# Kernel tuning notes

Hardware: AMD Instinct MI355X
Metric: run time of the kernel (lower is better)

The kernel has to match this reference:

```python
import jax, jax.numpy as jnp
import numpy as np

B, S, H, C = 8, 4096, 768, 64  # batch, seq_len, hidden_dim, block size


def _xavier(k, shape):
    fan = shape[0] + shape[1]
    return jax.random.normal(k, shape, jnp.float32) * np.sqrt(2.0 / fan)


def setup_inputs() -> dict:
    key = jax.random.key(0)
    kx, kq, kk, kv, k1, k2 = jax.random.split(key, 6)
    return {
        "x": jax.random.normal(kx, (B, S, H), jnp.float32),
        "Wq": _xavier(kq, (H, H)),
        "Wk": _xavier(kk, (H, H)),
        "Wv": _xavier(kv, (H, H)),
        "W1": _xavier(k1, (H, 16)),
        "W2": _xavier(k2, (16, H)),
        "b": jnp.zeros((H,), jnp.float32),
    }


def reference(x, Wq, Wk, Wv, W1, W2, b):
    Bb, Ss, Hh = x.shape
    NB = Ss // C  # number of blocks (seq_len divisible by C, no remainder)
    Q = x @ Wq
    K = x @ Wk
    V = x @ Wv
    # gating alpha: identical every block iteration in the original, compute once
    alpha = jax.nn.sigmoid((x @ W1) @ W2 + b) ** (1.0 / 16.0)  # [B,S,H]
    a = alpha.mean(axis=1, keepdims=True)  # [B,1,H], broadcasts over rows of state
    # blocks to leading axis for scan: [NB, B, C, H]
    qs = Q.reshape(Bb, NB, C, Hh).transpose(1, 0, 2, 3)
    ks = K.reshape(Bb, NB, C, Hh).transpose(1, 0, 2, 3)
    vs = V.reshape(Bb, NB, C, Hh).transpose(1, 0, 2, 3)
    mask = jnp.tril(jnp.ones((C, C), x.dtype))
    scale = 1.0 / np.sqrt(Hh).astype(np.float32)

    def step(St, blk):
        qb, kb, vb = blk  # each [B,C,H]
        # state update first (original updates S before computing output)
        St = St * a + jnp.einsum("bch,bcd->bhd", kb, vb)  # [B,H,H]
        # intra-block: scores masked by MULTIPLICATION (as in original), then softmax
        scores = jnp.einsum("bch,bdh->bcd", qb, kb) * mask * scale
        w = jax.nn.softmax(scores, axis=-1)
        out = jnp.einsum("bch,bhd->bcd", qb, St) + jnp.einsum("bcd,bde->bce", w, vb)
        return St, out

    S0 = jnp.zeros((Bb, Hh, Hh), x.dtype)
    _, outs = jax.lax.scan(step, S0, (qs, ks, vs))  # outs: [NB,B,C,H]
    O = outs.transpose(1, 0, 2, 3).reshape(Bb, Ss, Hh)
    return O
```

## Files before the change

kernel.cpp:

```cpp
#include <hip/hip_runtime.h>

#define B_ 8
#define S_ 4096
#define H_ 768
#define C_ 64
#define NB_ 64
#define M_ (B_*S_)

typedef _Float16 f16x8 __attribute__((ext_vector_type(8)));
typedef _Float16 f16x4 __attribute__((ext_vector_type(4)));
typedef float    f32x4 __attribute__((ext_vector_type(4)));

__global__ __launch_bounds__(256) void k_transpose(const float* __restrict__ src,
                                                   _Float16* __restrict__ dst) {
  __shared__ float tile[32][33];
  const int t = threadIdx.x;
  const int tx = t & 31, ty = t >> 5;
  const int n0 = blockIdx.x * 32, k0 = blockIdx.y * 32;
#pragma unroll
  for (int i = 0; i < 4; ++i)
    tile[ty + i*8][tx] = src[(k0 + ty + i*8) * H_ + n0 + tx];
  __syncthreads();
#pragma unroll
  for (int i = 0; i < 4; ++i)
    dst[(n0 + ty + i*8) * H_ + k0 + tx] = (_Float16)tile[tx][ty + i*8];
}

__global__ __launch_bounds__(256) void k_gemm_qkv(
    const float* __restrict__ x,
    const _Float16* __restrict__ WqT, const _Float16* __restrict__ WkT,
    const _Float16* __restrict__ WvT,
    _Float16* __restrict__ Qb, _Float16* __restrict__ Vb,
    _Float16* __restrict__ KT, _Float16* __restrict__ VT) {
  __shared__ _Float16 xs[64][40];
  __shared__ _Float16 ws[3][128][40];
  const int t = threadIdx.x;
  const int m0 = blockIdx.x * 64, n0 = blockIdx.y * 128;
  const int lane = t & 63, wv = t >> 6;
  const int lm = lane & 15, qd = lane >> 4;
  const int sm = t >> 2, sk = (t & 3) * 8;
  const int wn = t >> 1, wk = (t & 1) * 16;

  f32x4 acc[3][4][2];
#pragma unroll
  for (int a = 0; a < 3; ++a)
#pragma unroll
    for (int i = 0; i < 4; ++i)
#pragma unroll
      for (int n = 0; n < 2; ++n)
        acc[a][i][n] = (f32x4){0.f, 0.f, 0.f, 0.f};

  for (int kk = 0; kk < 24; ++kk) {
    const int k0 = kk * 32;
    __syncthreads();
    {
      const f32x4* xp = (const f32x4*)&x[(size_t)(m0 + sm) * H_ + k0 + sk];
      f32x4 f0 = xp[0], f1 = xp[1];
      f16x8 xv;
#pragma unroll
      for (int j = 0; j < 4; ++j) { xv[j] = (_Float16)f0[j]; xv[4 + j] = (_Float16)f1[j]; }
      *(f16x8*)&xs[sm][sk] = xv;
    }
    {
      const f16x8* wp = (const f16x8*)&WqT[(n0 + wn) * H_ + k0 + wk];
      *(f16x8*)&ws[0][wn][wk] = wp[0]; *(f16x8*)&ws[0][wn][wk + 8] = wp[1];
      wp = (const f16x8*)&WkT[(n0 + wn) * H_ + k0 + wk];
      *(f16x8*)&ws[1][wn][wk] = wp[0]; *(f16x8*)&ws[1][wn][wk + 8] = wp[1];
      wp = (const f16x8*)&WvT[(n0 + wn) * H_ + k0 + wk];
      *(f16x8*)&ws[2][wn][wk] = wp[0]; *(f16x8*)&ws[2][wn][wk + 8] = wp[1];
    }
    __syncthreads();
    f16x8 af[4];
#pragma unroll
    for (int i = 0; i < 4; ++i) af[i] = *(f16x8*)&xs[i*16 + lm][qd*8];
#pragma unroll
    for (int a = 0; a < 3; ++a)
#pragma unroll
      for (int n = 0; n < 2; ++n) {
        f16x8 bfr = *(f16x8*)&ws[a][wv*32 + n*16 + lm][qd*8];
#pragma unroll
        for (int i = 0; i < 4; ++i)
          acc[a][i][n] = __builtin_amdgcn_mfma_f32_16x16x32_f16(af[i], bfr, acc[a][i][n], 0, 0, 0);
      }
  }
#pragma unroll
  for (int i = 0; i < 4; ++i)
#pragma unroll
    for (int n = 0; n < 2; ++n) {
      const int ng = n0 + wv*32 + n*16 + lm;
      const int mg0 = m0 + i*16 + qd*4;
      const int bb = mg0 >> 12, ss = mg0 & (S_ - 1);
#pragma unroll
      for (int r = 0; r < 4; ++r) {
        Qb[(size_t)(mg0 + r) * H_ + ng] = (_Float16)acc[0][i][n][r];
        Vb[(size_t)(mg0 + r) * H_ + ng] = (_Float16)acc[2][i][n][r];
      }
      f16x4 kp, vp;
#pragma unroll
      for (int r = 0; r < 4; ++r) {
        kp[r] = (_Float16)acc[1][i][n][r];
        vp[r] = (_Float16)acc[2][i][n][r];
      }
      *(f16x4*)&KT[((size_t)bb * H_ + ng) * S_ + ss] = kp;
      *(f16x4*)&VT[((size_t)bb * H_ + ng) * S_ + ss] = vp;
    }
}

__global__ __launch_bounds__(256) void k_tgemm(const float* __restrict__ x,
                                               const float* __restrict__ W1,
                                               float* __restrict__ tbuf) {
  __shared__ float w1s[768 * 16];
  __shared__ float xs[64 * 129];
  const int t = threadIdx.x;
  const int m0 = blockIdx.x * 64;
  for (int i = t; i < 768 * 16 / 4; i += 256)
    ((f32x4*)w1s)[i] = ((const f32x4*)W1)[i];
  const int row = t & 63, cg = t >> 6;
  f32x4 acc = (f32x4){0.f, 0.f, 0.f, 0.f};
  for (int kc = 0; kc < 768; kc += 128) {
    __syncthreads();
    for (int i = 0; i < 32; ++i) {
      const int idx = t + 256 * i;
      const int r = idx >> 7, c = idx & 127;
      xs[r * 129 + c] = x[(size_t)(m0 + r) * H_ + kc + c];
    }
    __syncthreads();
#pragma unroll 8
    for (int kl = 0; kl < 128; ++kl) {
      const float a = xs[row * 129 + kl];
      const f32x4 w = *(const f32x4*)&w1s[(kc + kl) * 16 + cg * 4];
#pragma unroll
      for (int j = 0; j < 4; ++j) acc[j] += a * w[j];
    }
  }
  *(f32x4*)&tbuf[(size_t)(m0 + row) * 16 + cg * 4] = acc;
}

__global__ __launch_bounds__(256) void k_areduce(const float* __restrict__ tbuf,
                                                 const float* __restrict__ W2,
                                                 const float* __restrict__ bias,
                                                 float* __restrict__ abuf) {
  __shared__ float ts[128 * 17];
  __shared__ float rbuf[8 * 32];
  const int t = threadIdx.x;
  const int b = blockIdx.y, hc = blockIdx.x;
  const int hl = t & 31, sg = t >> 5;
  const int h = hc * 32 + hl;
  float w2r[16];
#pragma unroll
  for (int j = 0; j < 16; ++j) w2r[j] = W2[j * H_ + h];
  const float bb = bias[h];
  float asum = 0.f;
  const float* tb = &tbuf[(size_t)(b * S_) * 16];
  for (int sc = 0; sc < S_; sc += 128) {
    __syncthreads();
    for (int i = 0; i < 8; ++i) {
      const int idx = t + 256 * i;
      const int sl = idx >> 4, j = idx & 15;
      ts[sl * 17 + j] = tb[(size_t)(sc + sl) * 16 + j];
    }
    __syncthreads();
    for (int i = 0; i < 16; ++i) {
      const int sl = sg + i * 8;
      float z = bb;
      const float* tr = &ts[sl * 17];
#pragma unroll
      for (int j = 0; j < 16; ++j) z += tr[j] * w2r[j];
      const float sgm = 1.f / (1.f + __expf(-z));
      asum += sqrtf(sqrtf(sqrtf(sqrtf(sgm))));
    }
  }
  rbuf[sg * 32 + hl] = asum;
  __syncthreads();
  if (t < 32) {
    float s = 0.f;
#pragma unroll
    for (int g = 0; g < 8; ++g) s += rbuf[g * 32 + t];
    abuf[b * H_ + hc * 32 + t] = s * (1.f / (float)S_);
  }
}

__global__ __launch_bounds__(256) void k_scores_y(
    const _Float16* __restrict__ Qb, const _Float16* __restrict__ KT,
    const _Float16* __restrict__ Vb, float* __restrict__ O) {
  __shared__ float qs[64 * 68];
  __shared__ float ks[64 * 68];
  __shared__ float wb[64 * 68];
  __shared__ float vsb[64 * 68];
  const int t = threadIdx.x;
  const int nb = blockIdx.x, b = blockIdx.y;
  const size_t base = ((size_t)b * S_ + nb * 64) * H_;
  const int tc = t >> 4, td = t & 15;
  const int srow = t >> 2, sseg = (t & 3) * 16;

  float scr[4][4];
#pragma unroll
  for (int i = 0; i < 4; ++i)
#pragma unroll
    for (int u = 0; u < 4; ++u) scr[i][u] = 0.f;

  for (int hc = 0; hc < 12; ++hc) {
    __syncthreads();
    {
      const f16x8* qp = (const f16x8*)&Qb[base + (size_t)srow * H_ + hc * 64 + sseg];
      f16x8 q0 = qp[0], q1 = qp[1];
#pragma unroll
      for (int j = 0; j < 8; ++j) {
        qs[(sseg + j) * 68 + srow] = (float)q0[j];
        qs[(sseg + 8 + j) * 68 + srow] = (float)q1[j];
      }
    }
    {
      const size_t krow = ((size_t)b * H_ + hc * 64 + srow) * S_ + nb * 64 + sseg;
      f16x8 k0 = *(const f16x8*)&KT[krow];
      f16x8 k1 = *(const f16x8*)&KT[krow + 8];
      f32x4 f;
#pragma unroll
      for (int j = 0; j < 4; ++j) f[j] = (float)k0[j];
      *(f32x4*)&ks[srow * 68 + sseg] = f;
#pragma unroll
      for (int j = 0; j < 4; ++j) f[j] = (float)k0[4 + j];
      *(f32x4*)&ks[srow * 68 + sseg + 4] = f;
#pragma unroll
      for (int j = 0; j < 4; ++j) f[j] = (float)k1[j];
      *(f32x4*)&ks[srow * 68 + sseg + 8] = f;
#pragma unroll
      for (int j = 0; j < 4; ++j) f[j] = (float)k1[4 + j];
      *(f32x4*)&ks[srow * 68 + sseg + 12] = f;
    }
    __syncthreads();
#pragma unroll 4
    for (int h = 0; h < 64; ++h) {
      const f32x4 qv = *(f32x4*)&qs[h * 68 + tc * 4];
      const f32x4 kv = *(f32x4*)&ks[h * 68 + td * 4];
#pragma unroll
      for (int i = 0; i < 4; ++i)
#pragma unroll
        for (int u = 0; u < 4; ++u) scr[i][u] += qv[i] * kv[u];
    }
  }
  const float scale = 0.036084391824351615f;
#pragma unroll
  for (int i = 0; i < 4; ++i)
#pragma unroll
    for (int u = 0; u < 4; ++u) {
      const int c = tc * 4 + i, d = td * 4 + u;
      wb[d * 68 + c] = (d <= c) ? scr[i][u] * scale : 0.f;
    }
  __syncthreads();
  {
    const int r = t >> 2, g = t & 3;
    float vals[16];
    float mx = -1e30f;
#pragma unroll
    for (int i = 0; i < 16; ++i) {
      vals[i] = wb[(g * 16 + i) * 68 + r];
      mx = fmaxf(mx, vals[i]);
    }
    mx = fmaxf(mx, __shfl_xor(mx, 1));
    mx = fmaxf(mx, __shfl_xor(mx, 2));
    float sm = 0.f;
#pragma unroll
    for (int i = 0; i < 16; ++i) { vals[i] = __expf(vals[i] - mx); sm += vals[i]; }
    sm += __shfl_xor(sm, 1);
    sm += __shfl_xor(sm, 2);
    const float inv = 1.f / sm;
#pragma unroll
    for (int i = 0; i < 16; ++i) wb[(g * 16 + i) * 68 + r] = vals[i] * inv;
  }
  for (int ec = 0; ec < 12; ++ec) {
    __syncthreads();
    {
      const f16x8* vp = (const f16x8*)&Vb[base + (size_t)srow * H_ + ec * 64 + sseg];
      f16x8 v0 = vp[0], v1 = vp[1];
      f32x4 f;
#pragma unroll
      for (int j = 0; j < 4; ++j) f[j] = (float)v0[j];
      *(f32x4*)&vsb[srow * 68 + sseg] = f;
#pragma unroll
      for (int j = 0; j < 4; ++j) f[j] = (float)v0[4 + j];
      *(f32x4*)&vsb[srow * 68 + sseg + 4] = f;
#pragma unroll
      for (int j = 0; j < 4; ++j) f[j] = (float)v1[j];
      *(f32x4*)&vsb[srow * 68 + sseg + 8] = f;
#pragma unroll
      for (int j = 0; j < 4; ++j) f[j] = (float)v1[4 + j];
      *(f32x4*)&vsb[srow * 68 + sseg + 12] = f;
    }
    __syncthreads();
    float y[4][4];
#pragma unroll
    for (int i = 0; i < 4; ++i)
#pragma unroll
      for (int u = 0; u < 4; ++u) y[i][u] = 0.f;
#pragma unroll 4
    for (int j = 0; j < 64; ++j) {
      const f32x4 wv = *(f32x4*)&wb[j * 68 + tc * 4];
      const f32x4 vv = *(f32x4*)&vsb[j * 68 + td * 4];
#pragma unroll
      for (int i = 0; i < 4; ++i)
#pragma unroll
        for (int u = 0; u < 4; ++u) y[i][u] += wv[i] * vv[u];
    }
#pragma unroll
    for (int i = 0; i < 4; ++i) {
      f32x4 yv = {y[i][0], y[i][1], y[i][2], y[i][3]};
      *(f32x4*)&O[base + (size_t)(tc * 4 + i) * H_ + ec * 64 + td * 4] = yv;
    }
  }
}

#define STP 776
__global__ __launch_bounds__(256, 2) void k_scan(
    const _Float16* __restrict__ Qb, const _Float16* __restrict__ KT,
    const _Float16* __restrict__ VT, const float* __restrict__ abuf,
    float* __restrict__ O) {
  __shared__ _Float16 StL[32 * STP];
  const int t = threadIdx.x;
  const int b = blockIdx.y;
  const int d0 = blockIdx.x * 32;
  const int w = t >> 6, lane = t & 63;
  const int lm = lane & 15, qd = lane >> 4;

  const float av0 = abuf[b * H_ + d0 + lm];
  const float av1 = abuf[b * H_ + d0 + 16 + lm];

  f32x4 acc[12][2];
#pragma unroll
  for (int mt = 0; mt < 12; ++mt) {
    acc[mt][0] = (f32x4){0.f, 0.f, 0.f, 0.f};
    acc[mt][1] = (f32x4){0.f, 0.f, 0.f, 0.f};
  }

  const size_t ktb = (size_t)b * H_ * S_;
  const size_t vrow0 = ktb + (size_t)(d0 + lm) * S_;
  const size_t vrow1 = ktb + (size_t)(d0 + 16 + lm) * S_;

  for (int blk = 0; blk < NB_; ++blk) {
    const int s0 = blk * 64;
    f16x8 vf00 = *(const f16x8*)&VT[vrow0 + s0 + qd * 8];
    f16x8 vf01 = *(const f16x8*)&VT[vrow0 + s0 + 32 + qd * 8];
    f16x8 vf10 = *(const f16x8*)&VT[vrow1 + s0 + qd * 8];
    f16x8 vf11 = *(const f16x8*)&VT[vrow1 + s0 + 32 + qd * 8];
#pragma unroll
    for (int mt = 0; mt < 12; ++mt) {
      const size_t arow = ktb + (size_t)((w * 12 + mt) * 16 + lm) * S_ + s0 + qd * 8;
      f16x8 a0 = *(const f16x8*)&KT[arow];
      f16x8 a1 = *(const f16x8*)&KT[arow + 32];
      f32x4 c0 = acc[mt][0] * av0;
      f32x4 c1 = acc[mt][1] * av1;
      c0 = __builtin_amdgcn_mfma_f32_16x16x32_f16(a0, vf00, c0, 0, 0, 0);
      c0 = __builtin_amdgcn_mfma_f32_16x16x32_f16(a1, vf01, c0, 0, 0, 0);
      c1 = __builtin_amdgcn_mfma_f32_16x16x32_f16(a0, vf10, c1, 0, 0, 0);
      c1 = __builtin_amdgcn_mfma_f32_16x16x32_f16(a1, vf11, c1, 0, 0, 0);
      acc[mt][0] = c0;
      acc[mt][1] = c1;
    }
    __syncthreads();
#pragma unroll
    for (int mt = 0; mt < 12; ++mt) {
      const int h = (w * 12 + mt) * 16 + qd * 4;
      f16x4 p0, p1;
#pragma unroll
      for (int r = 0; r < 4; ++r) {
        p0[r] = (_Float16)acc[mt][0][r];
        p1[r] = (_Float16)acc[mt][1][r];
      }
      *(f16x4*)&StL[lm * STP + h] = p0;
      *(f16x4*)&StL[(16 + lm) * STP + h] = p1;
    }
    __syncthreads();
    f32x4 o0a = {0.f,0.f,0.f,0.f}, o0b = {0.f,0.f,0.f,0.f};
    f32x4 o1a = {0.f,0.f,0.f,0.f}, o1b = {0.f,0.f,0.f,0.f};
    const size_t qrow = ((size_t)b * S_ + s0 + w * 16 + lm) * H_ + qd * 8;
#pragma unroll 3
    for (int kt = 0; kt < 24; kt += 2) {
      f16x8 qa = *(const f16x8*)&Qb[qrow + kt * 32];
      f16x8 qb2 = *(const f16x8*)&Qb[qrow + kt * 32 + 32];
      f16x8 s00 = *(f16x8*)&StL[lm * STP + kt * 32 + qd * 8];
      f16x8 s01 = *(f16x8*)&StL[(16 + lm) * STP + kt * 32 + qd * 8];
      f16x8 s10 = *(f16x8*)&StL[lm * STP + kt * 32 + 32 + qd * 8];
      f16x8 s11 = *(f16x8*)&StL[(16 + lm) * STP + kt * 32 + 32 + qd * 8];
      o0a = __builtin_amdgcn_mfma_f32_16x16x32_f16(qa, s00, o0a, 0, 0, 0);
      o1a = __builtin_amdgcn_mfma_f32_16x16x32_f16(qa, s01, o1a, 0, 0, 0);
      o0b = __builtin_amdgcn_mfma_f32_16x16x32_f16(qb2, s10, o0b, 0, 0, 0);
      o1b = __builtin_amdgcn_mfma_f32_16x16x32_f16(qb2, s11, o1b, 0, 0, 0);
    }
    const f32x4 o0 = o0a + o0b;
    const f32x4 o1 = o1a + o1b;
    const size_t orow = ((size_t)b * S_ + s0 + w * 16 + qd * 4) * H_ + d0;
#pragma unroll
    for (int r = 0; r < 4; ++r) {
      O[orow + (size_t)r * H_ + lm] += o0[r];
      O[orow + (size_t)r * H_ + 16 + lm] += o1[r];
    }
  }
}

extern "C" void kernel_launch(void* const* d_in, const int* in_sizes, int n_in,
                              void* d_out, int out_size, void* d_ws, size_t ws_size,
                              hipStream_t stream) {
  (void)in_sizes; (void)n_in; (void)out_size; (void)ws_size;
  const float* x    = (const float*)d_in[0];
  const float* Wq   = (const float*)d_in[1];
  const float* Wk   = (const float*)d_in[2];
  const float* Wv   = (const float*)d_in[3];
  const float* W1   = (const float*)d_in[4];
  const float* W2   = (const float*)d_in[5];
  const float* bias = (const float*)d_in[6];
  float* O = (float*)d_out;

  char* ws = (char*)d_ws;
  _Float16* Qb  = (_Float16*)ws;
  _Float16* Vb  = Qb + (size_t)M_ * H_;
  _Float16* KT  = Vb + (size_t)M_ * H_;
  _Float16* VT  = KT + (size_t)M_ * H_;
  _Float16* WqT = VT + (size_t)M_ * H_;
  _Float16* WkT = WqT + H_ * H_;
  _Float16* WvT = WkT + H_ * H_;
  float* tbuf = (float*)(WvT + H_ * H_);
  float* abuf = tbuf + (size_t)M_ * 16;

  k_transpose<<<dim3(24, 24), 256, 0, stream>>>(Wq, WqT);
  k_transpose<<<dim3(24, 24), 256, 0, stream>>>(Wk, WkT);
  k_transpose<<<dim3(24, 24), 256, 0, stream>>>(Wv, WvT);
  k_gemm_qkv<<<dim3(512, 6), 256, 0, stream>>>(x, WqT, WkT, WvT, Qb, Vb, KT, VT);
  k_tgemm<<<dim3(512), 256, 0, stream>>>(x, W1, tbuf);
  k_areduce<<<dim3(24, 8), 256, 0, stream>>>(tbuf, W2, bias, abuf);
  k_scores_y<<<dim3(64, 8), 256, 0, stream>>>(Qb, KT, Vb, O);
  k_scan<<<dim3(24, 8), 256, 0, stream>>>(Qb, KT, VT, abuf, O);
}
```

Before: 1.534 ms.

## Split sequential state scan into parallel chunks with carry combine pass

The serial 64-block state scan, which ran on only 192 workgroups, is replaced by a three-phase chunked scan. Each of 8 chunks first computes its local state contribution in parallel. A combine kernel then propagates carries using a^8 decay, and a final pass recomputes each chunk's outputs starting from its carried-in state. This raises parallelism eightfold for the bottleneck kernel, at the cost of reading K and V twice and storing fp16 partial states. The row-major V copy is also dropped, and scores_y now reads and transposes from VT.

New measurement: 1.449 ms. 1.06x faster.

```diff
diff --git a/kernel.cpp b/kernel.cpp
--- a/kernel.cpp
+++ b/kernel.cpp
@@ -7,6 +7,9 @@
 #define NB_ 64
 #define M_ (B_*S_)
 
+#define NCH_ 8
+#define LCH_ 8
+
 typedef _Float16 f16x8 __attribute__((ext_vector_type(8)));
 typedef _Float16 f16x4 __attribute__((ext_vector_type(4)));
 typedef float    f32x4 __attribute__((ext_vector_type(4)));
@@ -30,7 +33,7 @@
     const float* __restrict__ x,
     const _Float16* __restrict__ WqT, const _Float16* __restrict__ WkT,
     const _Float16* __restrict__ WvT,
-    _Float16* __restrict__ Qb, _Float16* __restrict__ Vb,
+    _Float16* __restrict__ Qb,
     _Float16* __restrict__ KT, _Float16* __restrict__ VT) {
   __shared__ _Float16 xs[64][40];
   __shared__ _Float16 ws[3][128][40];
@@ -91,10 +94,8 @@
       const int mg0 = m0 + i*16 + qd*4;
       const int bb = mg0 >> 12, ss = mg0 & (S_ - 1);
 #pragma unroll
-      for (int r = 0; r < 4; ++r) {
+      for (int r = 0; r < 4; ++r)
         Qb[(size_t)(mg0 + r) * H_ + ng] = (_Float16)acc[0][i][n][r];
-        Vb[(size_t)(mg0 + r) * H_ + ng] = (_Float16)acc[2][i][n][r];
-      }
       f16x4 kp, vp;
 #pragma unroll
       for (int r = 0; r < 4; ++r) {
@@ -182,7 +183,7 @@
 
 __global__ __launch_bounds__(256) void k_scores_y(
     const _Float16* __restrict__ Qb, const _Float16* __restrict__ KT,
-    const _Float16* __restrict__ Vb, float* __restrict__ O) {
+    const _Float16* __restrict__ VT, float* __restrict__ O) {
   __shared__ float qs[64 * 68];
   __shared__ float ks[64 * 68];
   __shared__ float wb[64 * 68];
@@ -271,21 +272,14 @@
   for (int ec = 0; ec < 12; ++ec) {
     __syncthreads();
     {
-      const f16x8* vp = (const f16x8*)&Vb[base + (size_t)srow * H_ + ec * 64 + sseg];
-      f16x8 v0 = vp[0], v1 = vp[1];
-      f32x4 f;
-#pragma unroll
-      for (int j = 0; j < 4; ++j) f[j] = (float)v0[j];
-      *(f32x4*)&vsb[srow * 68 + sseg] = f;
-#pragma unroll
-      for (int j = 0; j < 4; ++j) f[j] = (float)v0[4 + j];
-      *(f32x4*)&vsb[srow * 68 + sseg + 4] = f;
-#pragma unroll
-      for (int j = 0; j < 4; ++j) f[j] = (float)v1[j];
-      *(f32x4*)&vsb[srow * 68 + sseg + 8] = f;
-#pragma unroll
-      for (int j = 0; j < 4; ++j) f[j] = (float)v1[4 + j];
-      *(f32x4*)&vsb[srow * 68 + sseg + 12] = f;
+      const size_t vrow = ((size_t)b * H_ + ec * 64 + srow) * S_ + nb * 64 + sseg;
+      f16x8 v0 = *(const f16x8*)&VT[vrow];
+      f16x8 v1 = *(const f16x8*)&VT[vrow + 8];
+#pragma unroll
+      for (int j = 0; j < 8; ++j) {
+        vsb[(sseg + j) * 68 + srow] = (float)v0[j];
+        vsb[(sseg + 8 + j) * 68 + srow] = (float)v1[j];
+      }
     }
     __syncthreads();
     float y[4][4];
@@ -310,15 +304,12 @@
   }
 }
 
-#define STP 776
-__global__ __launch_bounds__(256, 2) void k_scan(
-    const _Float16* __restrict__ Qb, const _Float16* __restrict__ KT,
-    const _Float16* __restrict__ VT, const float* __restrict__ abuf,
-    float* __restrict__ O) {
-  __shared__ _Float16 StL[32 * STP];
-  const int t = threadIdx.x;
-  const int b = blockIdx.y;
-  const int d0 = blockIdx.x * 32;
+__global__ __launch_bounds__(256, 2) void k_scan_chunk(
+    const _Float16* __restrict__ KT, const _Float16* __restrict__ VT,
+    const float* __restrict__ abuf, _Float16* __restrict__ Tb) {
+  const int t = threadIdx.x;
+  const int b = blockIdx.z, ch = blockIdx.y, dt = blockIdx.x;
+  const int d0 = dt * 32;
   const int w = t >> 6, lane = t & 63;
   const int lm = lane & 15, qd = lane >> 4;
 
@@ -336,7 +327,105 @@
   const size_t vrow0 = ktb + (size_t)(d0 + lm) * S_;
   const size_t vrow1 = ktb + (size_t)(d0 + 16 + lm) * S_;
 
-  for (int blk = 0; blk < NB_; ++blk) {
+  for (int blk = ch * LCH_; blk < ch * LCH_ + LCH_; ++blk) {
+    const int s0 = blk * 64;
+    f16x8 vf00 = *(const f16x8*)&VT[vrow0 + s0 + qd * 8];
+    f16x8 vf01 = *(const f16x8*)&VT[vrow0 + s0 + 32 + qd * 8];
+    f16x8 vf10 = *(const f16x8*)&VT[vrow1 + s0 + qd * 8];
+    f16x8 vf11 = *(const f16x8*)&VT[vrow1 + s0 + 32 + qd * 8];
+#pragma unroll
+    for (int mt = 0; mt < 12; ++mt) {
+      const size_t arow = ktb + (size_t)((w * 12 + mt) * 16 + lm) * S_ + s0 + qd * 8;
+      f16x8 a0 = *(const f16x8*)&KT[arow];
+      f16x8 a1 = *(const f16x8*)&KT[arow + 32];
+      f32x4 c0 = acc[mt][0] * av0;
+      f32x4 c1 = acc[mt][1] * av1;
+      c0 = __builtin_amdgcn_mfma_f32_16x16x32_f16(a0, vf00, c0, 0, 0, 0);
+      c0 = __builtin_amdgcn_mfma_f32_16x16x32_f16(a1, vf01, c0, 0, 0, 0);
+      c1 = __builtin_amdgcn_mfma_f32_16x16x32_f16(a0, vf10, c1, 0, 0, 0);
+      c1 = __builtin_amdgcn_mfma_f32_16x16x32_f16(a1, vf11, c1, 0, 0, 0);
+      acc[mt][0] = c0;
+      acc[mt][1] = c1;
+    }
+  }
+  _Float16* tp = Tb + ((((size_t)b * NCH_ + ch) * 24 + dt) * 32) * 768;
+#pragma unroll
+  for (int mt = 0; mt < 12; ++mt) {
+    const int h = (w * 12 + mt) * 16 + qd * 4;
+    f16x4 p0, p1;
+#pragma unroll
+    for (int r = 0; r < 4; ++r) {
+      p0[r] = (_Float16)acc[mt][0][r];
+      p1[r] = (_Float16)acc[mt][1][r];
+    }
+    *(f16x4*)&tp[(size_t)lm * 768 + h] = p0;
+    *(f16x4*)&tp[(size_t)(16 + lm) * 768 + h] = p1;
+  }
+}
+
+__global__ __launch_bounds__(256) void k_combine(const float* __restrict__ abuf,
+                                                 _Float16* __restrict__ Tb) {
+  const int gid = blockIdx.x * 256 + threadIdx.x;
+  const int hv = gid % 96;
+  const int dl = (gid / 96) & 31;
+  const int dt = (gid / (96 * 32)) % 24;
+  const int b  = gid / (96 * 32 * 24);
+  const float ad = abuf[b * H_ + dt * 32 + dl];
+  const float a2 = ad * ad, a4 = a2 * a2;
+  const float aL = a4 * a4;
+  float carry[8];
+#pragma unroll
+  for (int j = 0; j < 8; ++j) carry[j] = 0.f;
+  const size_t chstride = (size_t)24 * 32 * 768;
+  _Float16* p = Tb + (size_t)b * NCH_ * chstride + ((size_t)dt * 32 + dl) * 768 + hv * 8;
+  for (int ch = 0; ch < NCH_; ++ch, p += chstride) {
+    const f16x8 tv = *(const f16x8*)p;
+    f16x8 cv;
+#pragma unroll
+    for (int j = 0; j < 8; ++j) {
+      cv[j] = (_Float16)carry[j];
+      carry[j] = carry[j] * aL + (float)tv[j];
+    }
+    *(f16x8*)p = cv;
+  }
+}
+
+#define STP 776
+__global__ __launch_bounds__(256, 2) void k_scan_out(
+    const _Float16* __restrict__ Qb, const _Float16* __restrict__ KT,
+    const _Float16* __restrict__ VT, const float* __restrict__ abuf,
+    const _Float16* __restrict__ Tb, float* __restrict__ O) {
+  __shared__ _Float16 StL[32 * STP];
+  const int t = threadIdx.x;
+  const int b = blockIdx.z, ch = blockIdx.y, dt = blockIdx.x;
+  const int d0 = dt * 32;
+  const int w = t >> 6, lane = t & 63;
+  const int lm = lane & 15, qd = lane >> 4;
+
+  const float av0 = abuf[b * H_ + d0 + lm];
+  const float av1 = abuf[b * H_ + d0 + 16 + lm];
+
+  f32x4 acc[12][2];
+  {
+    const _Float16* tp = Tb + ((((size_t)b * NCH_ + ch) * 24 + dt) * 32) * 768;
+#pragma unroll
+    for (int mt = 0; mt < 12; ++mt) {
+      const int h = (w * 12 + mt) * 16 + qd * 4;
+      const f16x4 c0 = *(const f16x4*)&tp[(size_t)lm * 768 + h];
+      const f16x4 c1 = *(const f16x4*)&tp[(size_t)(16 + lm) * 768 + h];
+#pragma unroll
+      for (int r = 0; r < 4; ++r) {
+        acc[mt][0][r] = (float)c0[r];
+        acc[mt][1][r] = (float)c1[r];
+      }
+    }
+  }
+
+  const size_t ktb = (size_t)b * H_ * S_;
+  const size_t vrow0 = ktb + (size_t)(d0 + lm) * S_;
+  const size_t vrow1 = ktb + (size_t)(d0 + 16 + lm) * S_;
+
+  for (int blk = ch * LCH_; blk < ch * LCH_ + LCH_; ++blk) {
     const int s0 = blk * 64;
     f16x8 vf00 = *(const f16x8*)&VT[vrow0 + s0 + qd * 8];
     f16x8 vf01 = *(const f16x8*)&VT[vrow0 + s0 + 32 + qd * 8];
@@ -412,21 +501,23 @@
 
   char* ws = (char*)d_ws;
   _Float16* Qb  = (_Float16*)ws;
-  _Float16* Vb  = Qb + (size_t)M_ * H_;
-  _Float16* KT  = Vb + (size_t)M_ * H_;
+  _Float16* KT  = Qb + (size_t)M_ * H_;
   _Float16* VT  = KT + (size_t)M_ * H_;
   _Float16* WqT = VT + (size_t)M_ * H_;
   _Float16* WkT = WqT + H_ * H_;
   _Float16* WvT = WkT + H_ * H_;
   float* tbuf = (float*)(WvT + H_ * H_);
   float* abuf = tbuf + (size_t)M_ * 16;
+  _Float16* Tb = (_Float16*)(abuf + B_ * H_);
 
   k_transpose<<<dim3(24, 24), 256, 0, stream>>>(Wq, WqT);
   k_transpose<<<dim3(24, 24), 256, 0, stream>>>(Wk, WkT);
   k_transpose<<<dim3(24, 24), 256, 0, stream>>>(Wv, WvT);
-  k_gemm_qkv<<<dim3(512, 6), 256, 0, stream>>>(x, WqT, WkT, WvT, Qb, Vb, KT, VT);
+  k_gemm_qkv<<<dim3(512, 6), 256, 0, stream>>>(x, WqT, WkT, WvT, Qb, KT, VT);
   k_tgemm<<<dim3(512), 256, 0, stream>>>(x, W1, tbuf);
   k_areduce<<<dim3(24, 8), 256, 0, stream>>>(tbuf, W2, bias, abuf);
-  k_scores_y<<<dim3(64, 8), 256, 0, stream>>>(Qb, KT, Vb, O);
-  k_scan<<<dim3(24, 8), 256, 0, stream>>>(Qb, KT, VT, abuf, O);
-}
+  k_scores_y<<<dim3(64, 8), 256, 0, stream>>>(Qb, KT, VT, O);
+  k_scan_chunk<<<dim3(24, NCH_, 8), 256, 0, stream>>>(KT, VT, abuf, Tb);
+  k_combine<<<dim3(2304), 256, 0, stream>>>(abuf, Tb);
+  k_scan_out<<<dim3(24, NCH_, 8), 256, 0, stream>>>(Qb, KT, VT, abuf, Tb, O);
+}
```
